# Kernel tuning notes

Measured on AMD Instinct MI355X. Metric: run time of the kernel, lower is better.

The kernel has to match this reference:

```python
import jax, jax.numpy as jnp
import numpy as np
from jax import lax

KS = 10      # kernel_size (asserted == 10 in the torch module)
DCT_N = 10   # dct_n


def _dct_pair(N):
    k = np.arange(N)[:, None]
    i = np.arange(N)[None, :]
    w = np.full((N, 1), np.sqrt(2.0 / N))
    w[0, 0] = np.sqrt(1.0 / N)
    d = w * np.cos(np.pi * (i + 0.5) * k / N)
    return jnp.asarray(d, jnp.float32), jnp.asarray(np.linalg.inv(d), jnp.float32)


def _conv1d(x, w):
    # x: [B, C, L], w: [O, C, K], VALID conv (bias=False in torch)
    return lax.conv_general_dilated(x, w, (1,), 'VALID',
                                    dimension_numbers=('NCH', 'OIH', 'NCH'))


def _two_conv(x, w1, w2):
    return jax.nn.relu(_conv1d(jax.nn.relu(_conv1d(x, w1)), w2))


def _gconv(x, w, att, b):
    # GraphConvolution: att @ (x @ w) + b ; x: [B, node, f_in]
    return jnp.einsum('nm,bmo->bno', att, jnp.einsum('bmf,fo->bmo', x, w)) + b


def _gcn(x, gc1_w, gc1_att, gc1_b, gcb_w, gcb_att, gcb_b, gc7_w, gc7_att, gc7_b):
    # Standard motion-prediction GCN (eval mode: BN=identity, dropout off)
    y = jnp.tanh(_gconv(x, gc1_w, gc1_att, gc1_b))
    for s in range(gcb_w.shape[0]):  # small fixed num_stage
        h = jnp.tanh(_gconv(y, gcb_w[s, 0], gcb_att[s, 0], gcb_b[s, 0]))
        h = jnp.tanh(_gconv(h, gcb_w[s, 1], gcb_att[s, 1], gcb_b[s, 1]))
        y = y + h
    return _gconv(y, gc7_w, gc7_att, gc7_b) + x


def _ffc(x, wl, wg):
    # RealFFC(dim=3): spectral branch (rFFT over time, 1x1 conv on real/imag,
    # ReLU, irFFT) + local 1x1 branch. x: [B, 3, F/3, T]
    y = jnp.fft.rfft(x, axis=-1)
    yc = jnp.concatenate([y.real, y.imag], axis=1)            # [B, 6, F/3, K]
    yc = jax.nn.relu(jnp.einsum('oc,bcfk->bofk', wg, yc))
    re, im = jnp.split(yc, 2, axis=1)
    spec = jnp.fft.irfft(re + 1j * im, n=x.shape[-1], axis=-1)
    return jnp.einsum('oc,bcft->boft', wl, x) + spec


def _forward(input_seq, wq1, wq2, wk1, wk2,
             gc1_w, gc1_att, gc1_b, gcb_w, gcb_att, gcb_b,
             gc7_w, gc7_att, gc7_b, mlp_w1, mlp_w2, ffc_wl, ffc_wg,
             output_n, input_n):
    seq = input_seq[:, :input_n]
    B, _, F = seq.shape
    blen = KS + output_n                       # DCT block length (30)
    dctm, idctm = _dct_pair(blen)
    key_seq = jnp.swapaxes(seq, 1, 2)[:, :, :input_n - output_n]
    query_seq = jnp.swapaxes(seq, 1, 2)[:, :, -KS:]
    # im2col-style overlapping temporal blocks -> per-block DCT
    nvb = input_n - blen + 1
    idx = np.arange(blen)[None, :] + np.arange(nvb)[:, None]
    blocks = seq[:, idx]                       # [B, nvb, blen, F]
    # matches torch reshape(...,dct_n,-1).transpose(2,3).reshape: feature-major
    dvb = jnp.einsum('dk,bnkf->bnfd', dctm[:DCT_N], blocks).reshape(B, nvb, -1)
    key_feat = _two_conv(key_seq / 1000.0, wk1, wk2)       # [B, D, nvb]
    query_feat = _two_conv(query_seq / 1000.0, wq1, wq2)   # [B, D, 1]
    score = jnp.einsum('bdq,bdk->bqk', query_feat, key_feat) + 1e-15
    attn = score / jnp.sum(score, axis=2, keepdims=True)   # sum-normalized attention
    attended = jnp.einsum('bqk,bkf->bqf', attn, dvb)[:, 0].reshape(B, F, DCT_N)
    # FFC branch: pad with last frame x10, fold F into (3, F//3)
    ffc_in = jnp.concatenate([seq, jnp.repeat(seq[:, -1:], 10, axis=1)], axis=1)
    ffc_in = jnp.swapaxes(ffc_in, 1, 2).reshape(B, 3, F // 3, input_n + 10)
    ffc_out = _ffc(ffc_in, ffc_wl, ffc_wg).reshape(B, F, input_n + 10)[:, :, :DCT_N]
    ffc_out = jnp.swapaxes(ffc_out, 1, 2)      # [B, DCT_N, F]
    # GCN branch: last KS frames + last frame repeated output_n times
    gidx = np.concatenate([np.arange(input_n - KS, input_n),
                           np.full(output_n, input_n - 1)])
    gcn_in = seq[:, gidx]                      # [B, blen, F]
    dct_in = jnp.einsum('dk,bkf->bfd', dctm[:DCT_N], gcn_in)
    gcn_out = _gcn(dct_in, gc1_w, gc1_att, gc1_b, gcb_w, gcb_att, gcb_b,
                   gc7_w, gc7_att, gc7_b)      # [B, F, DCT_N]
    combined = jnp.concatenate([gcn_out, attended], axis=-1)
    recon = jnp.einsum('kd,bfd->bkf', idctm[:, :DCT_N], combined[:, :, :DCT_N])  # [B, blen, F]
    fused = jnp.swapaxes(jnp.concatenate([recon, ffc_out], axis=1), 1, 2)  # [B, F, blen+DCT_N=40]
    h = jax.nn.relu(jnp.einsum('bft,ot->bfo', fused, mlp_w1))  # Linear(40,256), no bias
    out = jnp.einsum('bfo,to->bft', h, mlp_w2)                 # Linear(256,40), no bias
    out = jnp.swapaxes(out, 1, 2)[:, :DCT_N]   # [B, DCT_N, F]
    return out[:, :, None, :]                  # [B, DCT_N, itera=1, F]


def setup_inputs() -> dict:
    key = jax.random.key(0)
    ks = jax.random.split(key, 20)
    B, T, F, D, NS = 1024, 50, 48, 512, 2
    p = lambda k, shp: jax.random.normal(k, shp, dtype=jnp.float32) * 0.05
    return {
        'input_seq': jax.random.normal(ks[0], (B, T, F), dtype=jnp.float32),
        'wq1': p(ks[1], (D, F, 6)), 'wq2': p(ks[2], (D, D, 5)),
        'wk1': p(ks[3], (D, F, 6)), 'wk2': p(ks[4], (D, D, 5)),
        'gc1_w': p(ks[5], (10, D)), 'gc1_att': p(ks[6], (F, F)), 'gc1_b': p(ks[7], (D,)),
        'gcb_w': p(ks[8], (NS, 2, D, D)), 'gcb_att': p(ks[9], (NS, 2, F, F)),
        'gcb_b': p(ks[10], (NS, 2, D)),
        'gc7_w': p(ks[11], (D, 10)), 'gc7_att': p(ks[12], (F, F)), 'gc7_b': p(ks[13], (10,)),
        'mlp_w1': p(ks[14], (256, 40)), 'mlp_w2': p(ks[15], (40, 256)),
        'ffc_wl': p(ks[16], (3, 3)), 'ffc_wg': p(ks[17], (6, 6)),
        'output_n': 20, 'input_n': 50, 'itera': 1,
    }


def reference(input_seq, wq1, wq2, wk1, wk2, gc1_w, gc1_att, gc1_b,
              gcb_w, gcb_att, gcb_b, gc7_w, gc7_att, gc7_b,
              mlp_w1, mlp_w2, ffc_wl, ffc_wg, output_n, input_n, itera):
    assert itera == 1  # single-iteration path (the torch itera>1 branch is skipped)
    return _forward(input_seq, wq1, wq2, wk1, wk2,
                    gc1_w, gc1_att, gc1_b, gcb_w, gcb_att, gcb_b,
                    gc7_w, gc7_att, gc7_b, mlp_w1, mlp_w2, ffc_wl, ffc_wg,
                    output_n, input_n)
```

## Files before the change

### kernel.cpp

```cpp
#include <hip/hip_runtime.h>
#include <math.h>

#define BB 1024
#define TT 50
#define FF 48
#define EXTN 60
#define NFREQ 31

typedef _Float16 h8 __attribute__((ext_vector_type(8)));
typedef _Float16 h4 __attribute__((ext_vector_type(4)));
typedef float f4 __attribute__((ext_vector_type(4)));

__device__ __forceinline__ float fast_tanh(float x) {
    float e = __expf(2.0f * x);
    return 1.0f - 2.0f * __builtin_amdgcn_rcpf(e + 1.0f);
}

__global__ void prep_kernel(const float* __restrict__ gcb_w, _Float16* __restrict__ P,
                            const float* __restrict__ gc1_w, _Float16* __restrict__ P1,
                            const float* __restrict__ gc7_w, _Float16* __restrict__ P7,
                            const float* __restrict__ mlp_w1, _Float16* __restrict__ Pw1,
                            const float* __restrict__ mlp_w2, _Float16* __restrict__ Pw2,
                            const float* __restrict__ gc1_att, const float* __restrict__ gcb_att,
                            const float* __restrict__ gc7_att, _Float16* __restrict__ attp,
                            _Float16* __restrict__ Pc_hi, _Float16* __restrict__ Pc_lo,
                            _Float16* __restrict__ Pi_hi, _Float16* __restrict__ Pi_lo,
                            float* __restrict__ dctm, float* __restrict__ dtail) {
    int blk = blockIdx.x, tid = threadIdx.x;
    const _Float16 HZ = (_Float16)0.0f;
    if (blk < 512) {
        int z = blk >> 7;
        int idx = ((blk & 127) << 8) | tid;
        int lane = idx & 63, t8 = idx >> 6;
        int nt = t8 & 7, kw = t8 >> 3;
        int ks = kw & 15, wv = kw >> 4;
        int n = wv * 128 + nt * 16 + (lane & 15);
        int k0 = ks * 32 + (lane >> 4) * 8;
        const float* src = gcb_w + (size_t)z * 262144 + n;
        h8 v;
        #pragma unroll
        for (int j = 0; j < 8; ++j) v[j] = (_Float16)src[(size_t)(k0 + j) * 512];
        *(h8*)(P + (size_t)z * 262144 + (size_t)idx * 8) = v;
    } else if (blk < 528) {
        int idx = ((blk - 512) << 8) | tid;
        int lane = idx & 63, t8 = idx >> 6;
        int nt = t8 & 7, kw = t8 >> 3;
        int ks = kw & 1, wv = kw >> 1;
        int n = wv * 128 + nt * 16 + (lane & 15);
        int k0 = ks * 32 + (lane >> 4) * 8;
        h8 v;
        #pragma unroll
        for (int j = 0; j < 8; ++j) v[j] = (k0 + j < 10) ? (_Float16)gc1_w[(k0 + j) * 512 + n] : HZ;
        *(h8*)(P1 + (size_t)idx * 8) = v;
    } else if (blk < 532) {
        int idx = ((blk - 528) << 8) | tid;
        int lane = idx & 63, t8 = idx >> 6;
        int ks = t8 & 3, wv = t8 >> 2;
        int n = lane & 15;
        int k0 = wv * 128 + ks * 32 + (lane >> 4) * 8;
        h8 v;
        #pragma unroll
        for (int j = 0; j < 8; ++j) v[j] = (n < 10) ? (_Float16)gc7_w[(k0 + j) * 10 + n] : HZ;
        *(h8*)(P7 + (size_t)idx * 8) = v;
    } else if (blk < 540) {
        int idx = ((blk - 532) << 8) | tid;
        int lane = idx & 63, t8 = idx >> 6;
        int ks = t8 & 1, q = t8 >> 1;
        int nt = q & 3, wv = q >> 2;
        int o = wv * 64 + nt * 16 + (lane & 15);
        int k0 = ks * 32 + (lane >> 4) * 8;
        h8 v;
        #pragma unroll
        for (int j = 0; j < 8; ++j) v[j] = (k0 + j < 40) ? (_Float16)mlp_w1[o * 40 + k0 + j] : HZ;
        *(h8*)(Pw1 + (size_t)idx * 8) = v;
    } else if (blk < 542) {
        int idx = ((blk - 540) << 8) | tid;
        int lane = idx & 63, ks = idx >> 6;
        int m = lane & 15;
        int k0 = ks * 32 + (lane >> 4) * 8;
        h8 v;
        #pragma unroll
        for (int j = 0; j < 8; ++j) v[j] = (m < 10) ? (_Float16)mlp_w2[m * 256 + k0 + j] : HZ;
        *(h8*)(Pw2 + (size_t)idx * 8) = v;
    } else if (blk < 614) {
        int idx = (blk - 542) * 256 + tid;
        if (idx < 18432) {
            int l = idx / 3072, r = (idx % 3072) / 64, m = idx & 63;
            float v = 0.f;
            if (m < 48) {
                v = (l == 0) ? gc1_att[r * 48 + m]
                  : (l <= 4) ? gcb_att[(l - 1) * 2304 + r * 48 + m]
                             : gc7_att[r * 48 + m];
            }
            attp[idx] = (_Float16)v;
        }
    } else if (blk < 646) {
        int g = (blk - 614) * 256 + tid;
        int tab = g >> 12, e = g & 4095;
        int j = e & 7, lane = (e >> 3) & 63, t8 = e >> 9;
        int ks = t8 & 1, nt = t8 >> 1;
        int n = nt * 16 + (lane & 15);
        int t = ks * 32 + (lane >> 4) * 8 + j;
        double v = 0.0;
        if (t < 60 && n < 62)
            v = (n < 31) ? cos(M_PI * (double)(n * t) / 30.0)
                         : -sin(M_PI * (double)((n - 31) * t) / 30.0);
        _Float16 hi = (_Float16)(float)v;
        if (tab == 0) Pc_hi[e] = hi;
        else          Pc_lo[e] = (_Float16)(float)(v - (double)(float)hi);
    } else if (blk < 654) {
        int g = (blk - 646) * 256 + tid;
        int tab = g >> 10, e = g & 1023;
        int j = e & 7, lane = (e >> 3) & 63, ks = e >> 9;
        int t = lane & 15;
        int kp = ks * 32 + (lane >> 4) * 8 + j;
        double v = 0.0;
        if (kp == 0) v = 1.0 / 60.0;
        else if (kp < 30) v = (2.0 / 60.0) * cos(M_PI * (double)(kp * t) / 30.0);
        else if (kp == 30) v = ((t & 1) ? -1.0 : 1.0) / 60.0;
        else if (kp >= 32 && kp < 61) v = -(2.0 / 60.0) * sin(M_PI * (double)((kp - 31) * t) / 30.0);
        _Float16 hi = (_Float16)(float)v;
        if (tab == 0) Pi_hi[e] = hi;
        else          Pi_lo[e] = (_Float16)(float)(v - (double)(float)hi);
    } else {
        int idx = (blk - 654) * 256 + tid;
        if (idx < 900) {
            int d = idx / 30, k = idx % 30;
            double w = (d == 0) ? sqrt(1.0 / 30.0) : sqrt(2.0 / 30.0);
            dctm[idx] = (float)(w * cos(M_PI * (k + 0.5) * d / 30.0));
        } else if (idx < 910) {
            int d = idx - 900;
            double w = (d == 0) ? sqrt(1.0 / 30.0) : sqrt(2.0 / 30.0);
            double s = 0.0;
            for (int k = 10; k < 30; ++k) s += w * cos(M_PI * (k + 0.5) * d / 30.0);
            dtail[d] = (float)s;
        }
    }
}

#define S_STRIDE 49152
#define RB_OFF   98304
#define G_OFF    (98304 + 26624)
#define DF_OFF   135168

template<int KSTEPS, int MODE>
__device__ __forceinline__ void gcn_layer(char* smem, char* T,
        const _Float16* __restrict__ Pw, const _Float16* __restrict__ attp,
        const float* __restrict__ bias, h4* sv,
        int lane, int wv8, int l16, int quad) {
    f4 acc[6][4];
    #pragma unroll
    for (int m = 0; m < 6; ++m)
        #pragma unroll
        for (int n = 0; n < 4; ++n) acc[m][n] = (f4)0.0f;

    const _Float16* Pb = Pw + (size_t)(wv8 >> 1) * (KSTEPS * 8 * 512)
                            + (size_t)(wv8 & 1) * 2048 + lane * 8;
    const int xm = l16 & 7;
    __syncthreads();

    #pragma unroll 2
    for (int ks = 0; ks < KSTEPS; ++ks) {
        h8 a[6], bfr[4];
        #pragma unroll
        for (int nt = 0; nt < 4; ++nt)
            bfr[nt] = *(const h8*)(Pb + (ks * 8 + nt) * 512);
        #pragma unroll
        for (int zz = 0; zz < 2; ++zz)
            #pragma unroll
            for (int mt = 0; mt < 3; ++mt)
                a[zz * 3 + mt] = *(h8*)(smem + zz * S_STRIDE + (mt * 16 + l16) * 1024
                                        + (((ks * 4 + quad) ^ xm) << 4));
        #pragma unroll
        for (int m = 0; m < 6; ++m)
            #pragma unroll
            for (int nt = 0; nt < 4; ++nt)
                acc[m][nt] = __builtin_amdgcn_mfma_f32_16x16x32_f16(a[m], bfr[nt], acc[m][nt], 0, 0, 0);
    }

    h8 ab[3][2];
    #pragma unroll
    for (int it = 0; it < 3; ++it)
        #pragma unroll
        for (int ks = 0; ks < 2; ++ks)
            ab[it][ks] = *(const h8*)(attp + (it * 16 + l16) * 64 + ks * 32 + quad * 8);

    __syncthreads();

    #pragma unroll
    for (int mt = 0; mt < 3; ++mt) {
        h4 hv;
        #pragma unroll
        for (int j = 0; j < 4; ++j) hv[j] = (_Float16)acc[mt][0][j];
        *(h4*)(T + l16 * 144 + (mt * 16 + quad * 4) * 2) = hv;
    }
    asm volatile("s_waitcnt lgkmcnt(0)" ::: "memory");
    h8 tf0 = *(h8*)(T + l16 * 144 + quad * 16);
    h8 tf1 = *(h8*)(T + l16 * 144 + 64 + quad * 16);

    #pragma unroll
    for (int e = 0; e < 8; ++e) {
        char* Tn = T + ((e + 1) & 1) * 2304;
        if (e < 7) {
            int zn = (e + 1) >> 2, nn = (e + 1) & 3;
            #pragma unroll
            for (int mt = 0; mt < 3; ++mt) {
                h4 hv;
                #pragma unroll
                for (int j = 0; j < 4; ++j) hv[j] = (_Float16)acc[zn * 3 + mt][nn][j];
                *(h4*)(Tn + l16 * 144 + (mt * 16 + quad * 4) * 2) = hv;
            }
        }
        f4 acc2[3];
        #pragma unroll
        for (int it = 0; it < 3; ++it) {
            acc2[it] = __builtin_amdgcn_mfma_f32_16x16x32_f16(tf0, ab[it][0], (f4)0.0f, 0, 0, 0);
            acc2[it] = __builtin_amdgcn_mfma_f32_16x16x32_f16(tf1, ab[it][1], acc2[it], 0, 0, 0);
        }
        if (e < 7) {
            asm volatile("s_waitcnt lgkmcnt(0)" ::: "memory");
            tf0 = *(h8*)(Tn + l16 * 144 + quad * 16);
            tf1 = *(h8*)(Tn + l16 * 144 + 64 + quad * 16);
        }
        const int z = e >> 2, nt = e & 3;
        const int c0 = wv8 * 64 + nt * 16 + quad * 4;
        const f4 bv = *(const f4*)(bias + c0);
        #pragma unroll
        for (int it = 0; it < 3; ++it) {
            int f = it * 16 + l16;
            char* sp = smem + z * S_STRIDE + f * 1024 + (((c0 >> 3) ^ (f & 7)) << 4) + ((c0 & 7) << 1);
            if (MODE == 1) sv[e * 3 + it] = *(h4*)sp;
            h4 o;
            #pragma unroll
            for (int j = 0; j < 4; ++j) {
                float v = fast_tanh(acc2[it][j] + bv[j]);
                if (MODE == 2) v += (float)sv[e * 3 + it][j];
                o[j] = (_Float16)v;
            }
            *(h4*)sp = o;
        }
    }
}

__launch_bounds__(512, 1)
__global__ void gcn_fused_kernel(const float* __restrict__ seq,
                                 const _Float16* __restrict__ P1,
                                 const _Float16* __restrict__ Pm,
                                 const _Float16* __restrict__ P7,
                                 const _Float16* __restrict__ attp,
                                 const float* __restrict__ gc1_b,
                                 const float* __restrict__ gcb_b,
                                 const float* __restrict__ gc7_b,
                                 const float* __restrict__ dctm,
                                 const float* __restrict__ dtail,
                                 _Float16* __restrict__ fush) {
    __shared__ __align__(16) char smem[139776];
    const int tid = threadIdx.x, lane = tid & 63, wv8 = tid >> 6;
    const int l16 = lane & 15, quad = lane >> 4;
    const int z = tid >> 8, ltid = tid & 255;
    const int b0 = blockIdx.x * 2;
    char* T = smem + RB_OFF + wv8 * 4608;

    {
        char* Rz = smem + RB_OFF + z * 4096;
        char* dctfz = smem + DF_OFF + z * 2304;
        const float* seqb = seq + (size_t)(b0 + z) * 2400;
        if (ltid < 120) *(f4*)(Rz + ltid * 16) = *(const f4*)(seqb + 1920 + ltid * 4);
        for (int v = ltid; v < 310; v += 256)
            ((float*)(Rz + 2048))[v] = (v < 300) ? dctm[v] : dtail[v - 300];
        __syncthreads();
        for (int v = ltid; v < 480; v += 256) {
            int f = v / 10, d = v % 10;
            const float* q = (const float*)Rz;
            const float* L = (const float*)(Rz + 2048);
            float a = L[300 + d] * q[9 * 48 + f];
            #pragma unroll
            for (int k = 0; k < 10; ++k) a += L[d * 30 + k] * q[k * 48 + f];
            ((float*)dctfz)[f * 12 + d] = a;
        }
        __syncthreads();
        for (int v = ltid; v < 384; v += 256) {
            int m = v >> 3, g = v & 7;
            h8 w = (h8)(_Float16)0.0f;
            if (g < 2) {
                #pragma unroll
                for (int j = 0; j < 8; ++j) {
                    int d = g * 8 + j;
                    if (d < 10) w[j] = (_Float16)((float*)dctfz)[m * 12 + d];
                }
            }
            *(h8*)(smem + z * S_STRIDE + m * 1024 + ((g ^ (m & 7)) << 4)) = w;
        }
        for (int v = tid; v < 768; v += 512) {
            int s = v % 3, rr = v / 3;
            int r = rr & 15, wb = rr >> 4;
            *(h8*)(smem + RB_OFF + wb * 2304 + r * 144 + 96 + s * 16) = (h8)(_Float16)0.0f;
        }
    }

    h4 sv[24];
    gcn_layer<2, 0>(smem, T, P1,          attp,          gc1_b,        sv, lane, wv8, l16, quad);
    gcn_layer<16, 1>(smem, T, Pm,          attp + 3072,  gcb_b,        sv, lane, wv8, l16, quad);
    gcn_layer<16, 2>(smem, T, Pm + 262144, attp + 6144,  gcb_b + 512,  sv, lane, wv8, l16, quad);
    gcn_layer<16, 1>(smem, T, Pm + 524288, attp + 9216,  gcb_b + 1024, sv, lane, wv8, l16, quad);
    gcn_layer<16, 2>(smem, T, Pm + 786432, attp + 12288, gcb_b + 1536, sv, lane, wv8, l16, quad);

    __syncthreads();
    {
        const int z6 = wv8 >> 2, wvl = wv8 & 3;
        char* Sz = smem + z6 * S_STRIDE;
        f4 acc[3];
        #pragma unroll
        for (int mt = 0; mt < 3; ++mt) acc[mt] = (f4)0.0f;
        const _Float16* Pb7 = P7 + wvl * 2048 + lane * 8;
        #pragma unroll
        for (int ks = 0; ks < 4; ++ks) {
            h8 bfr = *(const h8*)(Pb7 + ks * 512);
            int kh = wvl * 128 + ks * 32;
            #pragma unroll
            for (int mt = 0; mt < 3; ++mt) {
                h8 a = *(h8*)(Sz + (mt * 16 + l16) * 1024 + ((((kh >> 3) + quad) ^ (l16 & 7)) << 4));
                acc[mt] = __builtin_amdgcn_mfma_f32_16x16x32_f16(a, bfr, acc[mt], 0, 0, 0);
            }
        }
        #pragma unroll
        for (int mt = 0; mt < 3; ++mt)
            *(f4*)(smem + RB_OFF + z6 * 12288 + wvl * 3072 + l16 * 192 + (mt * 16 + quad * 4) * 4) = acc[mt];
    }
    __syncthreads();
    if ((wv8 & 3) == 0) {
        const int z6 = wv8 >> 2;
        char* PZ = smem + RB_OFF + z6 * 12288;
        char* dctfz = smem + DF_OFF + z6 * 2304;
        h4 tw[3]; int ns[3], ms[3];
        #pragma unroll
        for (int q = 0; q < 3; ++q) {
            int idx = lane * 3 + q;
            int n = idx / 12, m0 = (idx % 12) * 4;
            f4 s = *(f4*)(PZ + n * 192 + m0 * 4);
            s += *(f4*)(PZ + 3072 + n * 192 + m0 * 4);
            s += *(f4*)(PZ + 6144 + n * 192 + m0 * 4);
            s += *(f4*)(PZ + 9216 + n * 192 + m0 * 4);
            h4 h;
            #pragma unroll
            for (int j = 0; j < 4; ++j) h[j] = (_Float16)s[j];
            tw[q] = h; ns[q] = n; ms[q] = m0;
        }
        asm volatile("s_waitcnt lgkmcnt(0)" ::: "memory");
        #pragma unroll
        for (int q = 0; q < 3; ++q) *(h4*)(PZ + ns[q] * 144 + ms[q] * 2) = tw[q];
        if (lane < 48) {
            int row = lane / 3, s2 = lane % 3;
            *(h8*)(PZ + row * 144 + 96 + s2 * 16) = (h8)(_Float16)0.0f;
        }
        asm volatile("s_waitcnt lgkmcnt(0)" ::: "memory");
        h8 tf0 = *(h8*)(PZ + l16 * 144 + quad * 16);
        h8 tf1 = *(h8*)(PZ + l16 * 144 + 64 + quad * 16);
        const _Float16* a7 = attp + 15360;
        f4 acc2[3];
        #pragma unroll
        for (int it = 0; it < 3; ++it) {
            h8 ab0 = *(const h8*)(a7 + (it * 16 + l16) * 64 + quad * 8);
            h8 ab1 = *(const h8*)(a7 + (it * 16 + l16) * 64 + 32 + quad * 8);
            acc2[it] = __builtin_amdgcn_mfma_f32_16x16x32_f16(tf0, ab0, (f4)0.0f, 0, 0, 0);
            acc2[it] = __builtin_amdgcn_mfma_f32_16x16x32_f16(tf1, ab1, acc2[it], 0, 0, 0);
        }
        char* G = smem + G_OFF + z6 * 3072;
        #pragma unroll
        for (int it = 0; it < 3; ++it) {
            int f = it * 16 + l16;
            #pragma unroll
            for (int j = 0; j < 4; ++j) {
                int c = quad * 4 + j;
                if (c < 10) {
                    float v = acc2[it][j] + gc7_b[c] + ((float*)dctfz)[f * 12 + c];
                    *(float*)(G + f * 64 + c * 4) = v;
                }
            }
        }
    }
    __syncthreads();
    {
        char* G = smem + G_OFF + z * 3072;
        _Float16* fb = fush + (size_t)(b0 + z) * 3456;
        for (int v = ltid; v < 1440; v += 256) {
            int f = v / 30, t = v % 30;
            float s = 0.f;
            #pragma unroll
            for (int d = 0; d < 10; ++d) s += dctm[d * 30 + t] * *(float*)(G + f * 64 + d * 4);
            fb[f * 72 + t] = (_Float16)s;
        }
        for (int v = ltid; v < 1152; v += 256) {
            int f = v / 24, t = 40 + v % 24;
            fb[f * 72 + t] = (_Float16)0.0f;
        }
    }
}

__launch_bounds__(256, 3)
__global__ void ffc_mlp_kernel(const float* __restrict__ seq,
                               const _Float16* __restrict__ fush,
                               const float* __restrict__ wl,
                               const float* __restrict__ wg,
                               const _Float16* __restrict__ Pw1,
                               const _Float16* __restrict__ Pw2,
                               const _Float16* __restrict__ Pc_hi,
                               const _Float16* __restrict__ Pc_lo,
                               const _Float16* __restrict__ Pi_hi,
                               const _Float16* __restrict__ Pi_lo,
                               float* __restrict__ out) {
    __shared__ __align__(16) char smem[44736];
    float* ext     = (float*)smem;
    char*  extT_hi = smem + 11520;
    char*  extT_lo = smem + 18432;
    char*  Ya_hi   = extT_hi;
    char*  Ya_lo   = extT_lo;
    float* Xre     = (float*)(smem + 25344);
    float* Xim     = (float*)(smem + 31488);
    _Float16* fus  = (_Float16*)(smem + 37632);
    float* wls     = (float*)(smem + 44544);
    float* wgs     = (float*)(smem + 44580);
    _Float16* hlds = (_Float16*)smem;
    char*  R2      = smem + 25344;

    const int b = blockIdx.x, tid = threadIdx.x;
    const int lane = tid & 63, wv = tid >> 6;
    const int l16 = lane & 15, quad = lane >> 4;
    const float* s = seq + (size_t)b * TT * FF;

    for (int idx = tid; idx < EXTN * FF; idx += 256) {
        int t = idx / FF, f = idx % FF;
        ext[idx] = s[(t < TT ? t : TT - 1) * FF + f];
    }
    for (int idx = tid; idx < 64 * FF; idx += 256) {
        int t = idx / FF, f = idx % FF;
        float v = (t < EXTN) ? s[(t < TT ? t : TT - 1) * FF + f] : 0.f;
        _Float16 hi = (_Float16)v;
        ((_Float16*)(extT_hi + f * 144))[t] = hi;
        ((_Float16*)(extT_lo + f * 144))[t] = (_Float16)(v - (float)hi);
    }
    if (tid < 9) wls[tid] = wl[tid];
    if (tid >= 64 && tid < 100) wgs[tid - 64] = wg[tid - 64];
    __syncthreads();

    {
        const int nt = wv;
        f4 acc[3];
        #pragma unroll
        for (int mt = 0; mt < 3; ++mt) acc[mt] = (f4)0.0f;
        #pragma unroll
        for (int ks = 0; ks < 2; ++ks) {
            h8 bhi = *(const h8*)(Pc_hi + (nt * 2 + ks) * 512 + lane * 8);
            h8 blo = *(const h8*)(Pc_lo + (nt * 2 + ks) * 512 + lane * 8);
            #pragma unroll
            for (int mt = 0; mt < 3; ++mt) {
                h8 ahi = *(h8*)(extT_hi + (mt * 16 + l16) * 144 + ks * 64 + quad * 16);
                h8 alo = *(h8*)(extT_lo + (mt * 16 + l16) * 144 + ks * 64 + quad * 16);
                acc[mt] = __builtin_amdgcn_mfma_f32_16x16x32_f16(ahi, bhi, acc[mt], 0, 0, 0);
                acc[mt] = __builtin_amdgcn_mfma_f32_16x16x32_f16(alo, bhi, acc[mt], 0, 0, 0);
                acc[mt] = __builtin_amdgcn_mfma_f32_16x16x32_f16(ahi, blo, acc[mt], 0, 0, 0);
            }
        }
        int n = nt * 16 + l16;
        #pragma unroll
        for (int mt = 0; mt < 3; ++mt)
            #pragma unroll
            for (int i = 0; i < 4; ++i) {
                int f = mt * 16 + quad * 4 + i;
                if (n < 31) Xre[f * 32 + n] = acc[mt][i];
                else if (n < 62) Xim[f * 32 + n - 31] = acc[mt][i];
            }
    }
    for (int v = tid; v < 384; v += 256) {
        int f = v >> 3, g = v & 7;
        *(h8*)((char*)fus + f * 144 + g * 16) =
            *(const h8*)(fush + (size_t)b * 3456 + f * 72 + g * 8);
    }
    __syncthreads();

    for (int idx = tid; idx < 2976; idx += 256) {
        int k = idx % 31; int g = (idx / 31) % 16; int o = idx / (31 * 16);
        float v = wgs[o * 6 + 0] * Xre[g * 32 + k]        + wgs[o * 6 + 1] * Xre[(16 + g) * 32 + k]
                + wgs[o * 6 + 2] * Xre[(32 + g) * 32 + k] + wgs[o * 6 + 3] * Xim[g * 32 + k]
                + wgs[o * 6 + 4] * Xim[(16 + g) * 32 + k] + wgs[o * 6 + 5] * Xim[(32 + g) * 32 + k];
        v = fmaxf(v, 0.f);
        int fr = (o < 3) ? o * 16 + g : (o - 3) * 16 + g;
        int kp = (o < 3) ? k : 31 + k;
        _Float16 hi = (_Float16)v;
        ((_Float16*)(Ya_hi + fr * 144))[kp] = hi;
        ((_Float16*)(Ya_lo + fr * 144))[kp] = (_Float16)(v - (float)hi);
    }
    if (tid < 96) {
        int f = tid >> 1, c = 62 + (tid & 1);
        ((_Float16*)(Ya_hi + f * 144))[c] = (_Float16)0.0f;
        ((_Float16*)(Ya_lo + f * 144))[c] = (_Float16)0.0f;
    }
    __syncthreads();

    if (wv < 3) {
        const int mt = wv;
        f4 ac = (f4)0.0f;
        #pragma unroll
        for (int ks = 0; ks < 2; ++ks) {
            h8 bhi = *(const h8*)(Pi_hi + ks * 512 + lane * 8);
            h8 blo = *(const h8*)(Pi_lo + ks * 512 + lane * 8);
            h8 ahi = *(h8*)(Ya_hi + (mt * 16 + l16) * 144 + ks * 64 + quad * 16);
            h8 alo = *(h8*)(Ya_lo + (mt * 16 + l16) * 144 + ks * 64 + quad * 16);
            ac = __builtin_amdgcn_mfma_f32_16x16x32_f16(ahi, bhi, ac, 0, 0, 0);
            ac = __builtin_amdgcn_mfma_f32_16x16x32_f16(alo, bhi, ac, 0, 0, 0);
            ac = __builtin_amdgcn_mfma_f32_16x16x32_f16(ahi, blo, ac, 0, 0, 0);
        }
        int t = l16;
        if (t < 10) {
            #pragma unroll
            for (int i = 0; i < 4; ++i) {
                int g = quad * 4 + i;
                int f = mt * 16 + g;
                float loc = wls[mt * 3 + 0] * ext[t * FF + g]
                          + wls[mt * 3 + 1] * ext[t * FF + 16 + g]
                          + wls[mt * 3 + 2] * ext[t * FF + 32 + g];
                fus[f * 72 + 30 + t] = (_Float16)(ac[i] + loc);
            }
        }
    }
    __syncthreads();

    f4 acc1[3][4];
    #pragma unroll
    for (int mt = 0; mt < 3; ++mt)
        #pragma unroll
        for (int nt = 0; nt < 4; ++nt) acc1[mt][nt] = (f4)0.0f;
    #pragma unroll
    for (int ks = 0; ks < 2; ++ks) {
        h8 af[3], bf[4];
        #pragma unroll
        for (int mt = 0; mt < 3; ++mt)
            af[mt] = *(h8*)((char*)fus + (mt * 16 + l16) * 144 + ks * 64 + quad * 16);
        #pragma unroll
        for (int nt = 0; nt < 4; ++nt)
            bf[nt] = *(const h8*)(Pw1 + (size_t)(((wv * 4 + nt) * 2 + ks) * 512) + lane * 8);
        #pragma unroll
        for (int mt = 0; mt < 3; ++mt)
            #pragma unroll
            for (int nt = 0; nt < 4; ++nt)
                acc1[mt][nt] = __builtin_amdgcn_mfma_f32_16x16x32_f16(af[mt], bf[nt], acc1[mt][nt], 0, 0, 0);
    }
    __syncthreads();
    #pragma unroll
    for (int mt = 0; mt < 3; ++mt)
        #pragma unroll
        for (int nt = 0; nt < 4; ++nt) {
            int o = wv * 64 + nt * 16 + l16;
            #pragma unroll
            for (int j = 0; j < 4; ++j) {
                int f = mt * 16 + quad * 4 + j;
                hlds[f * 264 + o] = (_Float16)fmaxf(acc1[mt][nt][j], 0.f);
            }
        }
    __syncthreads();
    f4 acc2[3];
    #pragma unroll
    for (int nt3 = 0; nt3 < 3; ++nt3) acc2[nt3] = (f4)0.0f;
    #pragma unroll
    for (int ss = 0; ss < 2; ++ss) {
        int ks = wv * 2 + ss;
        h8 aw = *(const h8*)(Pw2 + (size_t)ks * 512 + lane * 8);
        #pragma unroll
        for (int nt3 = 0; nt3 < 3; ++nt3) {
            h8 bh = *(h8*)((char*)hlds + (nt3 * 16 + l16) * 528 + ks * 64 + quad * 16);
            acc2[nt3] = __builtin_amdgcn_mfma_f32_16x16x32_f16(aw, bh, acc2[nt3], 0, 0, 0);
        }
    }
    #pragma unroll
    for (int nt3 = 0; nt3 < 3; ++nt3)
        *(f4*)(R2 + wv * 3072 + (nt3 * 16 + l16) * 64 + quad * 16) = acc2[nt3];
    __syncthreads();
    for (int v = tid; v < 768; v += 256) {
        int f = v >> 4, t = v & 15;
        float sm = 0.f;
        #pragma unroll
        for (int w4 = 0; w4 < 4; ++w4) sm += *(float*)(R2 + w4 * 3072 + f * 64 + t * 4);
        if (t < 10) out[(size_t)b * 480 + t * 48 + f] = sm;
    }
}

extern "C" void kernel_launch(void* const* d_in, const int* in_sizes, int n_in,
                              void* d_out, int out_size, void* d_ws, size_t ws_size,
                              hipStream_t stream) {
    (void)in_sizes; (void)n_in; (void)out_size;
    const float* seq     = (const float*)d_in[0];
    const float* gc1_w   = (const float*)d_in[5];
    const float* gc1_att = (const float*)d_in[6];
    const float* gc1_b   = (const float*)d_in[7];
    const float* gcb_w   = (const float*)d_in[8];
    const float* gcb_att = (const float*)d_in[9];
    const float* gcb_b   = (const float*)d_in[10];
    const float* gc7_w   = (const float*)d_in[11];
    const float* gc7_att = (const float*)d_in[12];
    const float* gc7_b   = (const float*)d_in[13];
    const float* mlp_w1  = (const float*)d_in[14];
    const float* mlp_w2  = (const float*)d_in[15];
    const float* ffc_wl  = (const float*)d_in[16];
    const float* ffc_wg  = (const float*)d_in[17];
    float* out = (float*)d_out;
    char* ws = (char*)d_ws;

    float*    dctm  = (float*)ws;
    float*    dtail = dctm + 900;
    char*     p0    = ws + 4096;
    _Float16* Pm    = (_Float16*)p0;   p0 += 4 * 262144 * 2;
    _Float16* P1    = (_Float16*)p0;   p0 += 32768 * 2;
    _Float16* P7    = (_Float16*)p0;   p0 += 8192 * 2;
    _Float16* Pw1   = (_Float16*)p0;   p0 += 16384 * 2;
    _Float16* Pw2   = (_Float16*)p0;   p0 += 4096 * 2;
    _Float16* attp  = (_Float16*)p0;   p0 += 18432 * 2;
    _Float16* Pc_hi = (_Float16*)p0;   p0 += 4096 * 2;
    _Float16* Pc_lo = (_Float16*)p0;   p0 += 4096 * 2;
    _Float16* Pi_hi = (_Float16*)p0;   p0 += 1024 * 2;
    _Float16* Pi_lo = (_Float16*)p0;   p0 += 1024 * 2;
    const size_t fixed_bytes = (size_t)(p0 - ws);

    const size_t per_batch = 6912;
    size_t avail = (ws_size > fixed_bytes) ? (ws_size - fixed_bytes) : 0;
    int nc = 1;
    while ((size_t)(BB / nc) * per_batch > avail && nc < 64) nc *= 2;
    int Bc = BB / nc;
    _Float16* fush = (_Float16*)(ws + fixed_bytes);

    prep_kernel<<<658, 256, 0, stream>>>(gcb_w, Pm, gc1_w, P1, gc7_w, P7,
                                         mlp_w1, Pw1, mlp_w2, Pw2,
                                         gc1_att, gcb_att, gc7_att, attp,
                                         Pc_hi, Pc_lo, Pi_hi, Pi_lo, dctm, dtail);

    for (int ci = 0; ci < nc; ++ci) {
        const float* seqc = seq + (size_t)ci * Bc * TT * FF;
        float* outc = out + (size_t)ci * Bc * 480;
        gcn_fused_kernel<<<Bc / 2, 512, 0, stream>>>(seqc, P1, Pm, P7, attp,
                                                     gc1_b, gcb_b, gc7_b, dctm, dtail, fush);
        ffc_mlp_kernel<<<Bc, 256, 0, stream>>>(seqc, fush, ffc_wl, ffc_wg, Pw1, Pw2,
                                               Pc_hi, Pc_lo, Pi_hi, Pi_lo, outc);
    }
}
```

Baseline: 267.2 us.

## Stage GCN weight tiles into LDS with double-buffered global_load_lds

Weight fragments for each k-step are now copied directly from global memory into a double-buffered LDS region with global_load_lds, prefetching the next k-step while MFMAs run on the current one. Previously each wave read its weight fragments straight from global memory inside the MFMA loop. To free LDS for the 64KB weight buffer, the DCT feature scratch is spilled to a global workspace and re-read at the end, and the T-buffer zero padding moves into each layer. The cost is a block-wide barrier and a vmcnt wait every k-step, plus extra LDS and workspace use.

```diff
diff --git a/kernel.cpp b/kernel.cpp
--- a/kernel.cpp
+++ b/kernel.cpp
@@ -10,6 +10,9 @@
 typedef _Float16 h8 __attribute__((ext_vector_type(8)));
 typedef _Float16 h4 __attribute__((ext_vector_type(4)));
 typedef float f4 __attribute__((ext_vector_type(4)));
+
+#define AS1 __attribute__((address_space(1)))
+#define AS3 __attribute__((address_space(3)))
 
 __device__ __forceinline__ float fast_tanh(float x) {
     float e = __expf(2.0f * x);
@@ -139,32 +142,51 @@
 }
 
 #define S_STRIDE 49152
-#define RB_OFF   98304
+#define WB_OFF   98304
 #define G_OFF    (98304 + 26624)
-#define DF_OFF   135168
+
+template<int KSTEPS>
+__device__ __forceinline__ void stage_ks(const _Float16* __restrict__ Pw, char* wb,
+                                         int ks, int wv8, int lane) {
+    const char* g0 = (const char*)Pw + (size_t)ks * 8192 + lane * 16;
+    #pragma unroll
+    for (int i = 0; i < 4; ++i) {
+        int c = wv8 * 4 + i;
+        int p = c >> 3, sub = c & 7;
+        const char* g = g0 + (size_t)p * (KSTEPS * 8192) + sub * 1024;
+        char* l = wb + p * 8192 + sub * 1024;
+        __builtin_amdgcn_global_load_lds((const AS1 unsigned*)g, (AS3 unsigned*)l, 16, 0, 0);
+    }
+}
 
 template<int KSTEPS, int MODE>
-__device__ __forceinline__ void gcn_layer(char* smem, char* T,
+__device__ __forceinline__ void gcn_layer(char* smem,
         const _Float16* __restrict__ Pw, const _Float16* __restrict__ attp,
         const float* __restrict__ bias, h4* sv,
         int lane, int wv8, int l16, int quad) {
+    char* WB = smem + WB_OFF;
+    char* T  = WB + wv8 * 4608;
     f4 acc[6][4];
     #pragma unroll
     for (int m = 0; m < 6; ++m)
         #pragma unroll
         for (int n = 0; n < 4; ++n) acc[m][n] = (f4)0.0f;
-
-    const _Float16* Pb = Pw + (size_t)(wv8 >> 1) * (KSTEPS * 8 * 512)
-                            + (size_t)(wv8 & 1) * 2048 + lane * 8;
     const int xm = l16 & 7;
+
+    __syncthreads();
+    stage_ks<KSTEPS>(Pw, WB, 0, wv8, lane);
+    asm volatile("s_waitcnt vmcnt(0)" ::: "memory");
     __syncthreads();
 
     #pragma unroll 2
     for (int ks = 0; ks < KSTEPS; ++ks) {
-        h8 a[6], bfr[4];
+        if (ks + 1 < KSTEPS)
+            stage_ks<KSTEPS>(Pw, WB + ((ks + 1) & 1) * 32768, ks + 1, wv8, lane);
+        const char* Bp = WB + (ks & 1) * 32768 + (wv8 >> 1) * 8192 + (wv8 & 1) * 4096 + lane * 16;
+        h8 bfr[4], a[6];
         #pragma unroll
         for (int nt = 0; nt < 4; ++nt)
-            bfr[nt] = *(const h8*)(Pb + (ks * 8 + nt) * 512);
+            bfr[nt] = *(const h8*)(Bp + nt * 1024);
         #pragma unroll
         for (int zz = 0; zz < 2; ++zz)
             #pragma unroll
@@ -176,6 +198,9 @@
             #pragma unroll
             for (int nt = 0; nt < 4; ++nt)
                 acc[m][nt] = __builtin_amdgcn_mfma_f32_16x16x32_f16(a[m], bfr[nt], acc[m][nt], 0, 0, 0);
+        __builtin_amdgcn_sched_barrier(0);
+        asm volatile("s_waitcnt vmcnt(0)" ::: "memory");
+        __syncthreads();
     }
 
     h8 ab[3][2];
@@ -185,7 +210,11 @@
         for (int ks = 0; ks < 2; ++ks)
             ab[it][ks] = *(const h8*)(attp + (it * 16 + l16) * 64 + ks * 32 + quad * 8);
 
-    __syncthreads();
+    if (lane < 48) {
+        int row = lane / 3, s = lane % 3;
+        *(h8*)(T + row * 144 + 96 + s * 16) = (h8)(_Float16)0.0f;
+        *(h8*)(T + 2304 + row * 144 + 96 + s * 16) = (h8)(_Float16)0.0f;
+    }
 
     #pragma unroll
     for (int mt = 0; mt < 3; ++mt) {
@@ -253,17 +282,17 @@
                                  const float* __restrict__ gc7_b,
                                  const float* __restrict__ dctm,
                                  const float* __restrict__ dtail,
-                                 _Float16* __restrict__ fush) {
-    __shared__ __align__(16) char smem[139776];
+                                 _Float16* __restrict__ fush,
+                                 float* __restrict__ dctg) {
+    __shared__ __align__(16) char smem[163840];
     const int tid = threadIdx.x, lane = tid & 63, wv8 = tid >> 6;
     const int l16 = lane & 15, quad = lane >> 4;
     const int z = tid >> 8, ltid = tid & 255;
     const int b0 = blockIdx.x * 2;
-    char* T = smem + RB_OFF + wv8 * 4608;
 
     {
-        char* Rz = smem + RB_OFF + z * 4096;
-        char* dctfz = smem + DF_OFF + z * 2304;
+        char* Rz = smem + WB_OFF + z * 8192;
+        char* dctfz = Rz + 4096;
         const float* seqb = seq + (size_t)(b0 + z) * 2400;
         if (ltid < 120) *(f4*)(Rz + ltid * 16) = *(const f4*)(seqb + 1920 + ltid * 4);
         for (int v = ltid; v < 310; v += 256)
@@ -277,6 +306,7 @@
             #pragma unroll
             for (int k = 0; k < 10; ++k) a += L[d * 30 + k] * q[k * 48 + f];
             ((float*)dctfz)[f * 12 + d] = a;
+            dctg[(size_t)blockIdx.x * 1152 + z * 576 + f * 12 + d] = a;
         }
         __syncthreads();
         for (int v = ltid; v < 384; v += 256) {
@@ -291,19 +321,14 @@
             }
             *(h8*)(smem + z * S_STRIDE + m * 1024 + ((g ^ (m & 7)) << 4)) = w;
         }
-        for (int v = tid; v < 768; v += 512) {
-            int s = v % 3, rr = v / 3;
-            int r = rr & 15, wb = rr >> 4;
-            *(h8*)(smem + RB_OFF + wb * 2304 + r * 144 + 96 + s * 16) = (h8)(_Float16)0.0f;
-        }
     }
 
     h4 sv[24];
-    gcn_layer<2, 0>(smem, T, P1,          attp,          gc1_b,        sv, lane, wv8, l16, quad);
-    gcn_layer<16, 1>(smem, T, Pm,          attp + 3072,  gcb_b,        sv, lane, wv8, l16, quad);
-    gcn_layer<16, 2>(smem, T, Pm + 262144, attp + 6144,  gcb_b + 512,  sv, lane, wv8, l16, quad);
-    gcn_layer<16, 1>(smem, T, Pm + 524288, attp + 9216,  gcb_b + 1024, sv, lane, wv8, l16, quad);
-    gcn_layer<16, 2>(smem, T, Pm + 786432, attp + 12288, gcb_b + 1536, sv, lane, wv8, l16, quad);
+    gcn_layer<2, 0>(smem, P1,          attp,          gc1_b,        sv, lane, wv8, l16, quad);
+    gcn_layer<16, 1>(smem, Pm,          attp + 3072,  gcb_b,        sv, lane, wv8, l16, quad);
+    gcn_layer<16, 2>(smem, Pm + 262144, attp + 6144,  gcb_b + 512,  sv, lane, wv8, l16, quad);
+    gcn_layer<16, 1>(smem, Pm + 524288, attp + 9216,  gcb_b + 1024, sv, lane, wv8, l16, quad);
+    gcn_layer<16, 2>(smem, Pm + 786432, attp + 12288, gcb_b + 1536, sv, lane, wv8, l16, quad);
 
     __syncthreads();
     {
@@ -325,13 +350,12 @@
         }
         #pragma unroll
         for (int mt = 0; mt < 3; ++mt)
-            *(f4*)(smem + RB_OFF + z6 * 12288 + wvl * 3072 + l16 * 192 + (mt * 16 + quad * 4) * 4) = acc[mt];
+            *(f4*)(smem + WB_OFF + z6 * 12288 + wvl * 3072 + l16 * 192 + (mt * 16 + quad * 4) * 4) = acc[mt];
     }
     __syncthreads();
     if ((wv8 & 3) == 0) {
         const int z6 = wv8 >> 2;
-        char* PZ = smem + RB_OFF + z6 * 12288;
-        char* dctfz = smem + DF_OFF + z6 * 2304;
+        char* PZ = smem + WB_OFF + z6 * 12288;
         h4 tw[3]; int ns[3], ms[3];
         #pragma unroll
         for (int q = 0; q < 3; ++q) {
@@ -366,6 +390,7 @@
             acc2[it] = __builtin_amdgcn_mfma_f32_16x16x32_f16(tf1, ab1, acc2[it], 0, 0, 0);
         }
         char* G = smem + G_OFF + z6 * 3072;
+        const float* dfz = dctg + (size_t)blockIdx.x * 1152 + z6 * 576;
         #pragma unroll
         for (int it = 0; it < 3; ++it) {
             int f = it * 16 + l16;
@@ -373,7 +398,7 @@
             for (int j = 0; j < 4; ++j) {
                 int c = quad * 4 + j;
                 if (c < 10) {
-                    float v = acc2[it][j] + gc7_b[c] + ((float*)dctfz)[f * 12 + c];
+                    float v = acc2[it][j] + gc7_b[c] + dfz[f * 12 + c];
                     *(float*)(G + f * 64 + c * 4) = v;
                 }
             }
@@ -620,12 +645,13 @@
     _Float16* Pi_lo = (_Float16*)p0;   p0 += 1024 * 2;
     const size_t fixed_bytes = (size_t)(p0 - ws);
 
-    const size_t per_batch = 6912;
+    const size_t per_batch = 6912 + 2304;
     size_t avail = (ws_size > fixed_bytes) ? (ws_size - fixed_bytes) : 0;
     int nc = 1;
     while ((size_t)(BB / nc) * per_batch > avail && nc < 64) nc *= 2;
     int Bc = BB / nc;
     _Float16* fush = (_Float16*)(ws + fixed_bytes);
+    float*    dctg = (float*)(ws + fixed_bytes + (size_t)Bc * 6912);
 
     prep_kernel<<<658, 256, 0, stream>>>(gcb_w, Pm, gc1_w, P1, gc7_w, P7,
                                          mlp_w1, Pw1, mlp_w2, Pw2,
@@ -636,7 +662,8 @@
         const float* seqc = seq + (size_t)ci * Bc * TT * FF;
         float* outc = out + (size_t)ci * Bc * 480;
         gcn_fused_kernel<<<Bc / 2, 512, 0, stream>>>(seqc, P1, Pm, P7, attp,
-                                                     gc1_b, gcb_b, gc7_b, dctm, dtail, fush);
+                                                     gc1_b, gcb_b, gc7_b, dctm, dtail,
+                                                     fush, dctg);
         ffc_mlp_kernel<<<Bc, 256, 0, stream>>>(seqc, fush, ffc_wl, ffc_wg, Pw1, Pw2,
                                                Pc_hi, Pc_lo, Pi_hi, Pi_lo, outc);
     }
```

After: 287.9 us. 1.08x slower.

## Split GCN fused kernel across 16 waves instead of 8

Applied to the files above, without the earlier changes.

Doubles the GCN fused kernel's block size from 512 to 1024 threads, so each wave owns 32 output columns instead of 64. Per-wave accumulators shrink from 6x4 to 6x2 tiles, and the double-buffered transpose staging becomes a single buffer per wave. The final gc7 reduction now sums 8 partial slices instead of 4. The goal is more waves per CU to hide latency with fewer registers each, at the cost of more shared memory, more B-fragment loads relative to MFMA work, and an extra LDS wait on each of the serialized transpose steps.

```diff
diff --git a/kernel.cpp b/kernel.cpp
--- a/kernel.cpp
+++ b/kernel.cpp
@@ -139,32 +139,33 @@
 }
 
 #define S_STRIDE 49152
-#define RB_OFF   98304
-#define G_OFF    (98304 + 26624)
-#define DF_OFF   135168
+#define TR_OFF   98304
+#define DF_OFF   147456
+#define G_OFF    152064
 
 template<int KSTEPS, int MODE>
-__device__ __forceinline__ void gcn_layer(char* smem, char* T,
+__device__ __forceinline__ void gcn_layer(char* smem,
         const _Float16* __restrict__ Pw, const _Float16* __restrict__ attp,
         const float* __restrict__ bias, h4* sv,
-        int lane, int wv8, int l16, int quad) {
-    f4 acc[6][4];
+        int lane, int wv16, int l16, int quad) {
+    char* T = smem + TR_OFF + wv16 * 2304;
+    f4 acc[6][2];
     #pragma unroll
     for (int m = 0; m < 6; ++m)
         #pragma unroll
-        for (int n = 0; n < 4; ++n) acc[m][n] = (f4)0.0f;
-
-    const _Float16* Pb = Pw + (size_t)(wv8 >> 1) * (KSTEPS * 8 * 512)
-                            + (size_t)(wv8 & 1) * 2048 + lane * 8;
+        for (int n = 0; n < 2; ++n) acc[m][n] = (f4)0.0f;
+
+    const _Float16* Pb = Pw + (size_t)(wv16 >> 2) * (KSTEPS * 8 * 512)
+                            + (size_t)(wv16 & 3) * 1024 + lane * 8;
     const int xm = l16 & 7;
     __syncthreads();
 
     #pragma unroll 2
     for (int ks = 0; ks < KSTEPS; ++ks) {
-        h8 a[6], bfr[4];
-        #pragma unroll
-        for (int nt = 0; nt < 4; ++nt)
-            bfr[nt] = *(const h8*)(Pb + (ks * 8 + nt) * 512);
+        h8 a[6], bfr[2];
+        #pragma unroll
+        for (int nt = 0; nt < 2; ++nt)
+            bfr[nt] = *(const h8*)(Pb + ks * 4096 + nt * 512);
         #pragma unroll
         for (int zz = 0; zz < 2; ++zz)
             #pragma unroll
@@ -174,7 +175,7 @@
         #pragma unroll
         for (int m = 0; m < 6; ++m)
             #pragma unroll
-            for (int nt = 0; nt < 4; ++nt)
+            for (int nt = 0; nt < 2; ++nt)
                 acc[m][nt] = __builtin_amdgcn_mfma_f32_16x16x32_f16(a[m], bfr[nt], acc[m][nt], 0, 0, 0);
     }
 
@@ -188,42 +189,25 @@
     __syncthreads();
 
     #pragma unroll
-    for (int mt = 0; mt < 3; ++mt) {
-        h4 hv;
-        #pragma unroll
-        for (int j = 0; j < 4; ++j) hv[j] = (_Float16)acc[mt][0][j];
-        *(h4*)(T + l16 * 144 + (mt * 16 + quad * 4) * 2) = hv;
-    }
-    asm volatile("s_waitcnt lgkmcnt(0)" ::: "memory");
-    h8 tf0 = *(h8*)(T + l16 * 144 + quad * 16);
-    h8 tf1 = *(h8*)(T + l16 * 144 + 64 + quad * 16);
-
-    #pragma unroll
-    for (int e = 0; e < 8; ++e) {
-        char* Tn = T + ((e + 1) & 1) * 2304;
-        if (e < 7) {
-            int zn = (e + 1) >> 2, nn = (e + 1) & 3;
-            #pragma unroll
-            for (int mt = 0; mt < 3; ++mt) {
-                h4 hv;
-                #pragma unroll
-                for (int j = 0; j < 4; ++j) hv[j] = (_Float16)acc[zn * 3 + mt][nn][j];
-                *(h4*)(Tn + l16 * 144 + (mt * 16 + quad * 4) * 2) = hv;
-            }
-        }
+    for (int e = 0; e < 4; ++e) {
+        const int z = e >> 1, ntl = e & 1;
+        #pragma unroll
+        for (int mt = 0; mt < 3; ++mt) {
+            h4 hv;
+            #pragma unroll
+            for (int j = 0; j < 4; ++j) hv[j] = (_Float16)acc[z * 3 + mt][ntl][j];
+            *(h4*)(T + l16 * 144 + (mt * 16 + quad * 4) * 2) = hv;
+        }
+        asm volatile("s_waitcnt lgkmcnt(0)" ::: "memory");
+        h8 tf0 = *(h8*)(T + l16 * 144 + quad * 16);
+        h8 tf1 = *(h8*)(T + l16 * 144 + 64 + quad * 16);
         f4 acc2[3];
         #pragma unroll
         for (int it = 0; it < 3; ++it) {
             acc2[it] = __builtin_amdgcn_mfma_f32_16x16x32_f16(tf0, ab[it][0], (f4)0.0f, 0, 0, 0);
             acc2[it] = __builtin_amdgcn_mfma_f32_16x16x32_f16(tf1, ab[it][1], acc2[it], 0, 0, 0);
         }
-        if (e < 7) {
-            asm volatile("s_waitcnt lgkmcnt(0)" ::: "memory");
-            tf0 = *(h8*)(Tn + l16 * 144 + quad * 16);
-            tf1 = *(h8*)(Tn + l16 * 144 + 64 + quad * 16);
-        }
-        const int z = e >> 2, nt = e & 3;
-        const int c0 = wv8 * 64 + nt * 16 + quad * 4;
+        const int c0 = wv16 * 32 + ntl * 16 + quad * 4;
         const f4 bv = *(const f4*)(bias + c0);
         #pragma unroll
         for (int it = 0; it < 3; ++it) {
@@ -242,7 +226,7 @@
     }
 }
 
-__launch_bounds__(512, 1)
+__launch_bounds__(1024, 1)
 __global__ void gcn_fused_kernel(const float* __restrict__ seq,
                                  const _Float16* __restrict__ P1,
                                  const _Float16* __restrict__ Pm,
@@ -254,69 +238,68 @@
                                  const float* __restrict__ dctm,
                                  const float* __restrict__ dtail,
                                  _Float16* __restrict__ fush) {
-    __shared__ __align__(16) char smem[139776];
-    const int tid = threadIdx.x, lane = tid & 63, wv8 = tid >> 6;
+    __shared__ __align__(16) char smem[158208];
+    const int tid = threadIdx.x, lane = tid & 63, wv16 = tid >> 6;
     const int l16 = lane & 15, quad = lane >> 4;
-    const int z = tid >> 8, ltid = tid & 255;
+    const int z = tid >> 9, ltid = tid & 511;
     const int b0 = blockIdx.x * 2;
-    char* T = smem + RB_OFF + wv8 * 4608;
 
     {
-        char* Rz = smem + RB_OFF + z * 4096;
-        char* dctfz = smem + DF_OFF + z * 2304;
+        char* Rz = smem + TR_OFF + z * 8192;
+        float* dctfz = (float*)(smem + DF_OFF + z * 2304);
         const float* seqb = seq + (size_t)(b0 + z) * 2400;
         if (ltid < 120) *(f4*)(Rz + ltid * 16) = *(const f4*)(seqb + 1920 + ltid * 4);
-        for (int v = ltid; v < 310; v += 256)
+        for (int v = ltid; v < 310; v += 512)
             ((float*)(Rz + 2048))[v] = (v < 300) ? dctm[v] : dtail[v - 300];
         __syncthreads();
-        for (int v = ltid; v < 480; v += 256) {
+        for (int v = ltid; v < 480; v += 512) {
             int f = v / 10, d = v % 10;
             const float* q = (const float*)Rz;
             const float* L = (const float*)(Rz + 2048);
             float a = L[300 + d] * q[9 * 48 + f];
             #pragma unroll
             for (int k = 0; k < 10; ++k) a += L[d * 30 + k] * q[k * 48 + f];
-            ((float*)dctfz)[f * 12 + d] = a;
+            dctfz[f * 12 + d] = a;
         }
         __syncthreads();
-        for (int v = ltid; v < 384; v += 256) {
+        for (int v = ltid; v < 384; v += 512) {
             int m = v >> 3, g = v & 7;
             h8 w = (h8)(_Float16)0.0f;
             if (g < 2) {
                 #pragma unroll
                 for (int j = 0; j < 8; ++j) {
                     int d = g * 8 + j;
-                    if (d < 10) w[j] = (_Float16)((float*)dctfz)[m * 12 + d];
+                    if (d < 10) w[j] = (_Float16)dctfz[m * 12 + d];
                 }
             }
             *(h8*)(smem + z * S_STRIDE + m * 1024 + ((g ^ (m & 7)) << 4)) = w;
         }
-        for (int v = tid; v < 768; v += 512) {
+        for (int v = tid; v < 768; v += 1024) {
             int s = v % 3, rr = v / 3;
             int r = rr & 15, wb = rr >> 4;
-            *(h8*)(smem + RB_OFF + wb * 2304 + r * 144 + 96 + s * 16) = (h8)(_Float16)0.0f;
-        }
-    }
-
-    h4 sv[24];
-    gcn_layer<2, 0>(smem, T, P1,          attp,          gc1_b,        sv, lane, wv8, l16, quad);
-    gcn_layer<16, 1>(smem, T, Pm,          attp + 3072,  gcb_b,        sv, lane, wv8, l16, quad);
-    gcn_layer<16, 2>(smem, T, Pm + 262144, attp + 6144,  gcb_b + 512,  sv, lane, wv8, l16, quad);
-    gcn_layer<16, 1>(smem, T, Pm + 524288, attp + 9216,  gcb_b + 1024, sv, lane, wv8, l16, quad);
-    gcn_layer<16, 2>(smem, T, Pm + 786432, attp + 12288, gcb_b + 1536, sv, lane, wv8, l16, quad);
+            *(h8*)(smem + TR_OFF + wb * 2304 + r * 144 + 96 + s * 16) = (h8)(_Float16)0.0f;
+        }
+    }
+
+    h4 sv[12];
+    gcn_layer<2, 0>(smem, P1,          attp,          gc1_b,        sv, lane, wv16, l16, quad);
+    gcn_layer<16, 1>(smem, Pm,          attp + 3072,  gcb_b,        sv, lane, wv16, l16, quad);
+    gcn_layer<16, 2>(smem, Pm + 262144, attp + 6144,  gcb_b + 512,  sv, lane, wv16, l16, quad);
+    gcn_layer<16, 1>(smem, Pm + 524288, attp + 9216,  gcb_b + 1024, sv, lane, wv16, l16, quad);
+    gcn_layer<16, 2>(smem, Pm + 786432, attp + 12288, gcb_b + 1536, sv, lane, wv16, l16, quad);
 
     __syncthreads();
     {
-        const int z6 = wv8 >> 2, wvl = wv8 & 3;
+        const int z6 = wv16 >> 3, wvl = wv16 & 7;
         char* Sz = smem + z6 * S_STRIDE;
         f4 acc[3];
         #pragma unroll
         for (int mt = 0; mt < 3; ++mt) acc[mt] = (f4)0.0f;
-        const _Float16* Pb7 = P7 + wvl * 2048 + lane * 8;
-        #pragma unroll
-        for (int ks = 0; ks < 4; ++ks) {
-            h8 bfr = *(const h8*)(Pb7 + ks * 512);
-            int kh = wvl * 128 + ks * 32;
+        #pragma unroll
+        for (int ks = 0; ks < 2; ++ks) {
+            int c = wvl * 2 + ks;
+            h8 bfr = *(const h8*)(P7 + c * 512 + lane * 8);
+            int kh = c * 32;
             #pragma unroll
             for (int mt = 0; mt < 3; ++mt) {
                 h8 a = *(h8*)(Sz + (mt * 16 + l16) * 1024 + ((((kh >> 3) + quad) ^ (l16 & 7)) << 4));
@@ -325,22 +308,22 @@
         }
         #pragma unroll
         for (int mt = 0; mt < 3; ++mt)
-            *(f4*)(smem + RB_OFF + z6 * 12288 + wvl * 3072 + l16 * 192 + (mt * 16 + quad * 4) * 4) = acc[mt];
-    }
-    __syncthreads();
-    if ((wv8 & 3) == 0) {
-        const int z6 = wv8 >> 2;
-        char* PZ = smem + RB_OFF + z6 * 12288;
-        char* dctfz = smem + DF_OFF + z6 * 2304;
+            *(f4*)(smem + TR_OFF + (z6 * 8 + wvl) * 3072 + l16 * 192 + (mt * 16 + quad * 4) * 4) = acc[mt];
+    }
+    __syncthreads();
+    if ((wv16 & 7) == 0) {
+        const int z6 = wv16 >> 3;
+        char* PZ = smem + TR_OFF + z6 * 24576;
+        const float* dctfz = (const float*)(smem + DF_OFF + z6 * 2304);
         h4 tw[3]; int ns[3], ms[3];
         #pragma unroll
         for (int q = 0; q < 3; ++q) {
             int idx = lane * 3 + q;
             int n = idx / 12, m0 = (idx % 12) * 4;
             f4 s = *(f4*)(PZ + n * 192 + m0 * 4);
-            s += *(f4*)(PZ + 3072 + n * 192 + m0 * 4);
-            s += *(f4*)(PZ + 6144 + n * 192 + m0 * 4);
-            s += *(f4*)(PZ + 9216 + n * 192 + m0 * 4);
+            #pragma unroll
+            for (int sl = 1; sl < 8; ++sl)
+                s += *(f4*)(PZ + sl * 3072 + n * 192 + m0 * 4);
             h4 h;
             #pragma unroll
             for (int j = 0; j < 4; ++j) h[j] = (_Float16)s[j];
@@ -373,7 +356,7 @@
             for (int j = 0; j < 4; ++j) {
                 int c = quad * 4 + j;
                 if (c < 10) {
-                    float v = acc2[it][j] + gc7_b[c] + ((float*)dctfz)[f * 12 + c];
+                    float v = acc2[it][j] + gc7_b[c] + dctfz[f * 12 + c];
                     *(float*)(G + f * 64 + c * 4) = v;
                 }
             }
@@ -383,14 +366,14 @@
     {
         char* G = smem + G_OFF + z * 3072;
         _Float16* fb = fush + (size_t)(b0 + z) * 3456;
-        for (int v = ltid; v < 1440; v += 256) {
+        for (int v = ltid; v < 1440; v += 512) {
             int f = v / 30, t = v % 30;
             float s = 0.f;
             #pragma unroll
             for (int d = 0; d < 10; ++d) s += dctm[d * 30 + t] * *(float*)(G + f * 64 + d * 4);
             fb[f * 72 + t] = (_Float16)s;
         }
-        for (int v = ltid; v < 1152; v += 256) {
+        for (int v = ltid; v < 1152; v += 512) {
             int f = v / 24, t = 40 + v % 24;
             fb[f * 72 + t] = (_Float16)0.0f;
         }
@@ -635,8 +618,8 @@
     for (int ci = 0; ci < nc; ++ci) {
         const float* seqc = seq + (size_t)ci * Bc * TT * FF;
         float* outc = out + (size_t)ci * Bc * 480;
-        gcn_fused_kernel<<<Bc / 2, 512, 0, stream>>>(seqc, P1, Pm, P7, attp,
-                                                     gc1_b, gcb_b, gc7_b, dctm, dtail, fush);
+        gcn_fused_kernel<<<Bc / 2, 1024, 0, stream>>>(seqc, P1, Pm, P7, attp,
+                                                      gc1_b, gcb_b, gc7_b, dctm, dtail, fush);
         ffc_mlp_kernel<<<Bc, 256, 0, stream>>>(seqc, fush, ffc_wl, ffc_wg, Pw1, Pw2,
                                                Pc_hi, Pc_lo, Pi_hi, Pi_lo, outc);
     }
```

Result: slower. 279.1 us (+4.4%).
